# Kernel tuning notes

Hardware: AMD Instinct MI355X
Metric: run time of the kernel (lower is better)

The kernel has to match this reference:

```python
import jax, jax.numpy as jnp
import numpy as np

N = 50000      # num_nodes
E = 800000     # num_edges
D_IN = 128
D_HID = 128
D_EMB = 128
G = 4          # num_gcns
BN_EPS = 1e-5


def setup_inputs() -> dict:
    key = jax.random.key(0)
    ks = jax.random.split(key, 8)
    x = jax.random.normal(ks[0], (N, D_IN), dtype=jnp.float32)
    edge_index = jax.random.randint(ks[1], (2, E), 0, N, dtype=jnp.int64)
    # per-GCN params, stacked on leading G axis
    W1 = jax.random.normal(ks[2], (G, D_IN, D_HID), dtype=jnp.float32) / np.sqrt(D_IN)
    b1 = jnp.zeros((G, D_HID), dtype=jnp.float32)
    W2 = jax.random.normal(ks[3], (G, D_HID, D_EMB), dtype=jnp.float32) / np.sqrt(D_HID)
    b2 = jnp.zeros((G, D_EMB), dtype=jnp.float32)
    gamma1 = jnp.ones((G, D_HID), dtype=jnp.float32)
    beta1 = jnp.zeros((G, D_HID), dtype=jnp.float32)
    gamma2 = jnp.ones((G, D_EMB), dtype=jnp.float32)
    beta2 = jnp.zeros((G, D_EMB), dtype=jnp.float32)
    alpha = jnp.asarray(0.25, dtype=jnp.float32)  # PReLU (single shared param)
    mix_embed = jnp.full((N, G), 1.0 / G, dtype=jnp.float32)
    return {"x": x, "edge_index": edge_index, "W1": W1, "b1": b1, "W2": W2,
            "b2": b2, "gamma1": gamma1, "beta1": beta1, "gamma2": gamma2,
            "beta2": beta2, "alpha": alpha, "mix_embed": mix_embed}


def _gcn_norm(edge_index, num_nodes):
    # PyG GCNConv: add self-loops, symmetric normalization D^-1/2 (A+I) D^-1/2
    row, col = edge_index[0], edge_index[1]
    loop = jnp.arange(num_nodes, dtype=edge_index.dtype)
    row = jnp.concatenate([row, loop])
    col = jnp.concatenate([col, loop])
    w = jnp.ones(row.shape[0], dtype=jnp.float32)
    deg = jax.ops.segment_sum(w, col, num_segments=num_nodes)
    dinv = jnp.where(deg > 0, deg ** -0.5, 0.0)
    norm = dinv[row] * w * dinv[col]
    return row, col, norm


def _propagate(h, row, col, norm, num_nodes):
    # gather from source, scale by edge norm, scatter-add to target
    msg = h[row] * norm[:, None]
    return jax.ops.segment_sum(msg, col, num_segments=num_nodes)


def _batchnorm(z, gamma, beta):
    mu = jnp.mean(z, axis=0)
    var = jnp.mean((z - mu) ** 2, axis=0)  # biased, as torch BN training mode
    return (z - mu) * jax.lax.rsqrt(var + BN_EPS) * gamma + beta


def _prelu(z, alpha):
    return jnp.where(z > 0, z, alpha * z)


def reference(x, edge_index, W1, b1, W2, b2, gamma1, beta1, gamma2, beta2, alpha, mix_embed):
    num_nodes = x.shape[0]
    row, col, norm = _gcn_norm(edge_index, num_nodes)
    mix = jax.nn.softmax(mix_embed, axis=-1)  # [N, G]
    out = jnp.zeros((num_nodes, D_EMB), dtype=x.dtype)
    for g in range(G):  # small fixed number of mixture components
        h = x @ W1[g]
        z = _propagate(h, row, col, norm, num_nodes) + b1[g]
        z = _prelu(_batchnorm(z, gamma1[g], beta1[g]), alpha)
        h = z @ W2[g]
        z = _propagate(h, row, col, norm, num_nodes) + b2[g]
        z = _prelu(_batchnorm(z, gamma2[g], beta2[g]), alpha)
        out = out + mix[:, g:g + 1] * z
    return out
```

## Files before the change

kernel.cpp:

```cpp
#include <hip/hip_runtime.h>
#include <stdint.h>

static constexpr float EPS = 1e-5f;

typedef __attribute__((ext_vector_type(8))) short bfrag;
typedef __attribute__((ext_vector_type(4))) float ffrag;

__device__ __forceinline__ float bf2f(unsigned short u){
  union { unsigned int i; float f; } v; v.i = ((unsigned int)u) << 16; return v.f;
}
__device__ __forceinline__ unsigned short f2bf(float f){
  union { float f; unsigned int i; } v; v.f = f;
  unsigned int x = v.i;
  x += 0x7fffu + ((x >> 16) & 1u);
  return (unsigned short)(x >> 16);
}
__device__ __forceinline__ float lo16(unsigned int v){ return bf2f((unsigned short)(v & 0xffffu)); }
__device__ __forceinline__ float hi16(unsigned int v){ return bf2f((unsigned short)(v >> 16)); }
__device__ __forceinline__ unsigned int pack2(float a, float b){
  return ((unsigned int)f2bf(b) << 16) | (unsigned int)f2bf(a);
}

__global__ void k_deg(const int* __restrict__ col, int* __restrict__ indeg, int N, int E){
  int e = blockIdx.x * 256 + threadIdx.x;
  if (e < E){
    unsigned c = (unsigned)col[e];
    if (c < (unsigned)N) atomicAdd(&indeg[c], 1);
  }
}

__global__ void k_blocksum(const int* __restrict__ indeg, int* __restrict__ bsum, int N){
  __shared__ int sm[256];
  int i = blockIdx.x * 256 + threadIdx.x;
  sm[threadIdx.x] = (i < N) ? indeg[i] : 0;
  __syncthreads();
  for (int d = 128; d > 0; d >>= 1){
    if (threadIdx.x < d) sm[threadIdx.x] += sm[threadIdx.x + d];
    __syncthreads();
  }
  if (threadIdx.x == 0) bsum[blockIdx.x] = sm[0];
}

__global__ void k_scan_bsum(int* bsum, int nb){
  if (threadIdx.x == 0 && blockIdx.x == 0){
    int acc = 0;
    for (int b = 0; b < nb; b++){ int v = bsum[b]; bsum[b] = acc; acc += v; }
  }
}

__global__ void k_scan_node(const int* __restrict__ indeg, const int* __restrict__ bsum,
                            int* __restrict__ offs, int* __restrict__ cursor,
                            float* __restrict__ dinv, int N){
  __shared__ int sm[256];
  int i = blockIdx.x * 256 + threadIdx.x;
  int v = (i < N) ? indeg[i] : 0;
  sm[threadIdx.x] = v;
  __syncthreads();
  for (int d = 1; d < 256; d <<= 1){
    int t = (threadIdx.x >= d) ? sm[threadIdx.x - d] : 0;
    __syncthreads();
    sm[threadIdx.x] += t;
    __syncthreads();
  }
  if (i < N){
    int o = bsum[blockIdx.x] + sm[threadIdx.x] - v;
    offs[i] = o; cursor[i] = o;
    dinv[i] = rsqrtf((float)(v + 1));
  }
}

__global__ void k_scatter(const int* __restrict__ row, const int* __restrict__ col,
                          int* __restrict__ cursor, int* __restrict__ csr, int N, int E){
  int e = blockIdx.x * 256 + threadIdx.x;
  if (e < E){
    unsigned c = (unsigned)col[e];
    if (c < (unsigned)N){
      int p = atomicAdd(&cursor[c], 1);
      unsigned r = (unsigned)row[e];
      csr[p] = (r < (unsigned)N) ? (int)r : 0;
    }
  }
}

__global__ void k_wcast(const float* __restrict__ W, unsigned short* __restrict__ Wt, int total){
  int idx = blockIdx.x * 256 + threadIdx.x;
  if (idx < total){
    int c = idx >> 7, k = idx & 127;
    int g = c >> 7, j = c & 127;
    Wt[idx] = f2bf(W[(size_t)g*16384 + k*128 + j]);
  }
}

__global__ void k_castx(const float* __restrict__ x, const float* __restrict__ dinv,
                        unsigned short* __restrict__ xs, int total4){
  int idx = blockIdx.x * 256 + threadIdx.x;
  int stride = gridDim.x * 256;
  for (; idx < total4; idx += stride){
    int i = idx >> 5;
    float di = dinv[i];
    float4 v = ((const float4*)x)[idx];
    ushort4 o;
    o.x = f2bf(di * v.x); o.y = f2bf(di * v.y);
    o.z = f2bf(di * v.z); o.w = f2bf(di * v.w);
    ((ushort4*)xs)[idx] = o;
  }
}

__global__ __launch_bounds__(64) void k_prop_x(const unsigned int* __restrict__ xs2,
                                               const int* __restrict__ csr,
                                               const int* __restrict__ offs, const int* __restrict__ indeg,
                                               const float* __restrict__ dinv,
                                               unsigned int* __restrict__ s2, int N){
  int i = blockIdx.x;
  int c2 = threadIdx.x;
  unsigned int sv = xs2[(size_t)i*64 + c2];
  float ax = lo16(sv), ay = hi16(sv);
  int e = offs[i], end = e + indeg[i];
  for (; e + 4 <= end; e += 4){
    int r0 = csr[e], r1 = csr[e+1], r2 = csr[e+2], r3 = csr[e+3];
    unsigned int v0 = xs2[(size_t)r0*64 + c2];
    unsigned int v1 = xs2[(size_t)r1*64 + c2];
    unsigned int v2 = xs2[(size_t)r2*64 + c2];
    unsigned int v3 = xs2[(size_t)r3*64 + c2];
    ax += lo16(v0) + lo16(v1) + lo16(v2) + lo16(v3);
    ay += hi16(v0) + hi16(v1) + hi16(v2) + hi16(v3);
  }
  for (; e < end; e++){
    unsigned int v = xs2[(size_t)csr[e]*64 + c2];
    ax += lo16(v); ay += hi16(v);
  }
  float di = dinv[i];
  s2[(size_t)i*64 + c2] = pack2(di * ax, di * ay);
}

__global__ __launch_bounds__(256) void k_mm_mfma(const unsigned short* __restrict__ in,
                                                 const unsigned short* __restrict__ Wt,
                                                 const float* __restrict__ bias,
                                                 unsigned short* __restrict__ out,
                                                 int N, int in_stride, int kmul){
  int wave = threadIdx.x >> 6;
  int lane = threadIdx.x & 63;
  int l16 = lane & 15, quad = lane >> 4;
  int node = blockIdx.x * 16 + l16;
  int nc = node < N ? node : N - 1;
  int colbase0 = wave * 128;
  int kofs = kmul * wave;

  const unsigned short* inrow = in + (size_t)nc * in_stride + kofs + quad * 8;
  bfrag b0 = *(const bfrag*)(inrow);
  bfrag b1 = *(const bfrag*)(inrow + 32);
  bfrag b2 = *(const bfrag*)(inrow + 64);
  bfrag b3 = *(const bfrag*)(inrow + 96);

  #pragma unroll
  for (int ct = 0; ct < 8; ct++){
    int colbase = colbase0 + ct * 16;
    const unsigned short* wrow = Wt + (size_t)(colbase + l16) * 128 + quad * 8;
    bfrag a0 = *(const bfrag*)(wrow);
    bfrag a1 = *(const bfrag*)(wrow + 32);
    bfrag a2 = *(const bfrag*)(wrow + 64);
    bfrag a3 = *(const bfrag*)(wrow + 96);
    ffrag acc = {0.f, 0.f, 0.f, 0.f};
    acc = __builtin_amdgcn_mfma_f32_16x16x32_bf16(a0, b0, acc, 0, 0, 0);
    acc = __builtin_amdgcn_mfma_f32_16x16x32_bf16(a1, b1, acc, 0, 0, 0);
    acc = __builtin_amdgcn_mfma_f32_16x16x32_bf16(a2, b2, acc, 0, 0, 0);
    acc = __builtin_amdgcn_mfma_f32_16x16x32_bf16(a3, b3, acc, 0, 0, 0);
    float4 bb = *(const float4*)(bias + colbase + quad * 4);
    uint2 o;
    o.x = pack2(acc[0] + bb.x, acc[1] + bb.y);
    o.y = pack2(acc[2] + bb.z, acc[3] + bb.w);
    if (node < N)
      *(uint2*)(out + (size_t)node * 512 + colbase + quad * 4) = o;
  }
}

__global__ __launch_bounds__(256) void k_stats(const unsigned int* __restrict__ z2,
                                               float* __restrict__ ssum, float* __restrict__ ssq, int N){
  int t = threadIdx.x;
  int rpb = (N + gridDim.x - 1) / gridDim.x;
  int r0 = blockIdx.x * rpb;
  int r1 = min(N, r0 + rpb);
  float s0 = 0.f, q0 = 0.f, s1 = 0.f, q1 = 0.f;
  for (int r = r0; r < r1; r++){
    unsigned int v = z2[(size_t)r * 256 + t];
    float a = lo16(v), b = hi16(v);
    s0 += a; q0 += a * a; s1 += b; q1 += b * b;
  }
  atomicAdd(&ssum[2 * t], s0);     atomicAdd(&ssq[2 * t], q0);
  atomicAdd(&ssum[2 * t + 1], s1); atomicAdd(&ssq[2 * t + 1], q1);
}

__global__ void k_bnfix(const float* __restrict__ ssum, const float* __restrict__ ssq,
                        const float* __restrict__ gamma, const float* __restrict__ beta,
                        float* __restrict__ scale, float* __restrict__ shift, int N){
  int c = blockIdx.x * 256 + threadIdx.x;
  if (c < 512){
    float mean = ssum[c] / (float)N;
    float var  = ssq[c] / (float)N - mean * mean;
    float rstd = rsqrtf(var + EPS);
    float sc = rstd * gamma[c];
    scale[c] = sc;
    shift[c] = beta[c] - mean * sc;
  }
}

__global__ void k_h(const unsigned short* __restrict__ z, const float* __restrict__ scale,
                    const float* __restrict__ shift, const float* __restrict__ alpha_p,
                    const float* __restrict__ dinv,
                    unsigned short* __restrict__ h, int total4){
  float alpha = alpha_p[0];
  int idx = blockIdx.x * 256 + threadIdx.x;
  int stride = gridDim.x * 256;
  for (; idx < total4; idx += stride){
    ushort4 u = ((const ushort4*)z)[idx];
    int c4 = idx & 127;
    int i  = idx >> 7;
    float di = dinv[i];
    float4 sc = ((const float4*)scale)[c4];
    float4 sh = ((const float4*)shift)[c4];
    float a0 = bf2f(u.x)*sc.x + sh.x; a0 = a0 > 0.f ? a0 : alpha*a0;
    float a1 = bf2f(u.y)*sc.y + sh.y; a1 = a1 > 0.f ? a1 : alpha*a1;
    float a2 = bf2f(u.z)*sc.z + sh.z; a2 = a2 > 0.f ? a2 : alpha*a2;
    float a3 = bf2f(u.w)*sc.w + sh.w; a3 = a3 > 0.f ? a3 : alpha*a3;
    ushort4 o; o.x = f2bf(di*a0); o.y = f2bf(di*a1); o.z = f2bf(di*a2); o.w = f2bf(di*a3);
    ((ushort4*)h)[idx] = o;
  }
}

__global__ __launch_bounds__(256) void k_prop_h(const unsigned int* __restrict__ h2,
                                                const int* __restrict__ csr,
                                                const int* __restrict__ offs, const int* __restrict__ indeg,
                                                const float* __restrict__ dinv,
                                                unsigned int* __restrict__ t2, int N){
  int i = blockIdx.x;
  int c2 = threadIdx.x;
  unsigned int sv = h2[(size_t)i*256 + c2];
  float ax = lo16(sv), ay = hi16(sv);
  int e = offs[i], end = e + indeg[i];
  for (; e + 4 <= end; e += 4){
    int r0 = csr[e], r1 = csr[e+1], r2 = csr[e+2], r3 = csr[e+3];
    unsigned int v0 = h2[(size_t)r0*256 + c2];
    unsigned int v1 = h2[(size_t)r1*256 + c2];
    unsigned int v2 = h2[(size_t)r2*256 + c2];
    unsigned int v3 = h2[(size_t)r3*256 + c2];
    ax += lo16(v0) + lo16(v1) + lo16(v2) + lo16(v3);
    ay += hi16(v0) + hi16(v1) + hi16(v2) + hi16(v3);
  }
  for (; e < end; e++){
    unsigned int v = h2[(size_t)csr[e]*256 + c2];
    ax += lo16(v); ay += hi16(v);
  }
  float di = dinv[i];
  t2[(size_t)i*256 + c2] = pack2(di * ax, di * ay);
}

__global__ void k_out(const unsigned short* __restrict__ z2, const float* __restrict__ scale,
                      const float* __restrict__ shift, const float* __restrict__ mixe,
                      const float* __restrict__ alpha_p, float* __restrict__ out, int N){
  float alpha = alpha_p[0];
  int idx = blockIdx.x * 256 + threadIdx.x;
  if (idx >= N * 128) return;
  int i = idx >> 7, j = idx & 127;
  float4 me = ((const float4*)mixe)[i];
  float mx = fmaxf(fmaxf(me.x, me.y), fmaxf(me.z, me.w));
  float e0 = __expf(me.x - mx), e1 = __expf(me.y - mx), e2 = __expf(me.z - mx), e3 = __expf(me.w - mx);
  float inv = 1.f / (e0 + e1 + e2 + e3);
  float r = 0.f;
  #pragma unroll
  for (int g = 0; g < 4; g++){
    int c = g * 128 + j;
    float v = bf2f(z2[(size_t)i*512 + c]) * scale[c] + shift[c];
    v = v > 0.f ? v : alpha * v;
    float m = (g == 0) ? e0 : (g == 1) ? e1 : (g == 2) ? e2 : e3;
    r += m * inv * v;
  }
  out[idx] = r;
}

extern "C" void kernel_launch(void* const* d_in, const int* in_sizes, int n_in,
                              void* d_out, int out_size, void* d_ws, size_t ws_size,
                              hipStream_t stream) {
  const float* x      = (const float*)d_in[0];
  const int*   ei     = (const int*)d_in[1];
  const float* W1     = (const float*)d_in[2];
  const float* b1     = (const float*)d_in[3];
  const float* W2     = (const float*)d_in[4];
  const float* b2     = (const float*)d_in[5];
  const float* gamma1 = (const float*)d_in[6];
  const float* beta1  = (const float*)d_in[7];
  const float* gamma2 = (const float*)d_in[8];
  const float* beta2  = (const float*)d_in[9];
  const float* alpha  = (const float*)d_in[10];
  const float* mixe   = (const float*)d_in[11];
  float* out = (float*)d_out;

  const int N = in_sizes[0] / 128;
  const int E = in_sizes[1] / 2;
  const int* rowv = ei;
  const int* colv = ei + E;

  char* w = (char*)d_ws;
  size_t off = 0;
  auto take = [&](size_t bytes) -> void* {
    void* p = w + off;
    off = (off + bytes + 255) & ~(size_t)255;
    return p;
  };
  int*   indeg  = (int*)take((size_t)N * 4);
  int*   cursor = (int*)take((size_t)N * 4);
  int*   offs   = (int*)take((size_t)N * 4);
  int*   bsum   = (int*)take(4096);
  float* dinv   = (float*)take((size_t)N * 4);
  float* sum1   = (float*)take(2048);
  float* sq1    = (float*)take(2048);
  float* sum2   = (float*)take(2048);
  float* sq2    = (float*)take(2048);
  float* scale1 = (float*)take(2048);
  float* shift1 = (float*)take(2048);
  float* scale2 = (float*)take(2048);
  float* shift2 = (float*)take(2048);
  int*   csr    = (int*)take((size_t)E * 4);
  unsigned short* Wt1 = (unsigned short*)take(512 * 128 * 2);
  unsigned short* Wt2 = (unsigned short*)take(512 * 128 * 2);
  unsigned short* xs = (unsigned short*)take((size_t)N * 128 * 2);
  unsigned short* sb = (unsigned short*)take((size_t)N * 128 * 2);
  unsigned short* z  = (unsigned short*)take((size_t)N * 512 * 2);
  unsigned short* h  = (unsigned short*)take((size_t)N * 512 * 2);
  unsigned short* z2 = (unsigned short*)take((size_t)N * 512 * 2);

  hipMemsetAsync(indeg, 0, (size_t)N * 4, stream);
  hipMemsetAsync(sum1, 0, 4 * 2048, stream);

  int ebl = (E + 255) / 256;
  int nb  = (N + 255) / 256;

  k_deg<<<ebl, 256, 0, stream>>>(colv, indeg, N, E);
  k_blocksum<<<nb, 256, 0, stream>>>(indeg, bsum, N);
  k_scan_bsum<<<1, 64, 0, stream>>>(bsum, nb);
  k_scan_node<<<nb, 256, 0, stream>>>(indeg, bsum, offs, cursor, dinv, N);
  k_scatter<<<ebl, 256, 0, stream>>>(rowv, colv, cursor, csr, N, E);

  k_wcast<<<256, 256, 0, stream>>>(W1, Wt1, 512 * 128);
  k_wcast<<<256, 256, 0, stream>>>(W2, Wt2, 512 * 128);

  k_castx<<<512, 256, 0, stream>>>(x, dinv, xs, N * 32);
  k_prop_x<<<N, 64, 0, stream>>>((const unsigned int*)xs, csr, offs, indeg, dinv, (unsigned int*)sb, N);

  int mmb = (N + 15) / 16;
  k_mm_mfma<<<mmb, 256, 0, stream>>>(sb, Wt1, b1, z, N, 128, 0);
  k_stats<<<512, 256, 0, stream>>>((const unsigned int*)z, sum1, sq1, N);
  k_bnfix<<<2, 256, 0, stream>>>(sum1, sq1, gamma1, beta1, scale1, shift1, N);
  k_h<<<2048, 256, 0, stream>>>(z, scale1, shift1, alpha, dinv, h, N * 128);
  k_prop_h<<<N, 256, 0, stream>>>((const unsigned int*)h, csr, offs, indeg, dinv, (unsigned int*)z, N);
  k_mm_mfma<<<mmb, 256, 0, stream>>>(z, Wt2, b2, z2, N, 512, 128);
  k_stats<<<512, 256, 0, stream>>>((const unsigned int*)z2, sum2, sq2, N);
  k_bnfix<<<2, 256, 0, stream>>>(sum2, sq2, gamma2, beta2, scale2, shift2, N);
  k_out<<<(N * 128 + 255) / 256, 256, 0, stream>>>(z2, scale2, shift2, mixe, alpha, out, N);
}
```

Baseline: 624.1 us.

## Compute BatchNorm stats via input Gram matrices and fuse BN/PReLU into matmuls

BatchNorm statistics of z = s@W are now derived from the Gram matrix sᵀs and the column means of the propagated input, computed with MFMA, instead of materialising z and reducing over it. This lets the first matmul apply BN, PReLU and the dinv scale directly in its epilogue. The second matmul likewise fuses BN, PReLU and the softmax mixture sum into its epilogue, which removes the z/z2 intermediate buffers and the separate stats, h and out kernels. It also parallelises the block-offset scan, merges the two weight casts into one launch, packs four nodes per block in the x propagation, and unrolls the gather loops by 8. The trade-off is fp32 atomics on Gram matrices from only 32 blocks per group, and variance computed as E[x²]−mean², which is less numerically robust. Biases are dropped, which is exact here because BN removes any constant shift.

After: 600.9 us. -3.7%, faster.

```diff
diff --git a/kernel.cpp b/kernel.cpp
--- a/kernel.cpp
+++ b/kernel.cpp
@@ -41,11 +41,19 @@
   if (threadIdx.x == 0) bsum[blockIdx.x] = sm[0];
 }
 
-__global__ void k_scan_bsum(int* bsum, int nb){
-  if (threadIdx.x == 0 && blockIdx.x == 0){
-    int acc = 0;
-    for (int b = 0; b < nb; b++){ int v = bsum[b]; bsum[b] = acc; acc += v; }
-  }
+__global__ __launch_bounds__(1024) void k_scan_bsum(int* bsum, int nb){
+  __shared__ int sm[1024];
+  int t = threadIdx.x;
+  int v = (t < nb) ? bsum[t] : 0;
+  sm[t] = v;
+  __syncthreads();
+  for (int d = 1; d < 1024; d <<= 1){
+    int u = (t >= d) ? sm[t - d] : 0;
+    __syncthreads();
+    sm[t] += u;
+    __syncthreads();
+  }
+  if (t < nb) bsum[t] = sm[t] - v;
 }
 
 __global__ void k_scan_node(const int* __restrict__ indeg, const int* __restrict__ bsum,
@@ -82,13 +90,14 @@
   }
 }
 
-__global__ void k_wcast(const float* __restrict__ W, unsigned short* __restrict__ Wt, int total){
+__global__ void k_wcast(const float* __restrict__ W1, const float* __restrict__ W2,
+                        unsigned short* __restrict__ Wt1, unsigned short* __restrict__ Wt2){
   int idx = blockIdx.x * 256 + threadIdx.x;
-  if (idx < total){
-    int c = idx >> 7, k = idx & 127;
-    int g = c >> 7, j = c & 127;
-    Wt[idx] = f2bf(W[(size_t)g*16384 + k*128 + j]);
-  }
+  const float* W = W1; unsigned short* Wt = Wt1;
+  if (idx >= 65536){ idx -= 65536; W = W2; Wt = Wt2; }
+  int c = idx >> 7, k = idx & 127;
+  int g = c >> 7, j = c & 127;
+  Wt[(size_t)c * 128 + k] = f2bf(W[(size_t)g*16384 + k*128 + j]);
 }
 
 __global__ void k_castx(const float* __restrict__ x, const float* __restrict__ dinv,
@@ -106,24 +115,26 @@
   }
 }
 
-__global__ __launch_bounds__(64) void k_prop_x(const unsigned int* __restrict__ xs2,
+__global__ __launch_bounds__(256) void k_prop_x(const unsigned int* __restrict__ xs2,
                                                const int* __restrict__ csr,
                                                const int* __restrict__ offs, const int* __restrict__ indeg,
                                                const float* __restrict__ dinv,
                                                unsigned int* __restrict__ s2, int N){
-  int i = blockIdx.x;
-  int c2 = threadIdx.x;
+  int i = blockIdx.x * 4 + (threadIdx.x >> 6);
+  if (i >= N) return;
+  int c2 = threadIdx.x & 63;
   unsigned int sv = xs2[(size_t)i*64 + c2];
   float ax = lo16(sv), ay = hi16(sv);
   int e = offs[i], end = e + indeg[i];
-  for (; e + 4 <= end; e += 4){
+  for (; e + 8 <= end; e += 8){
     int r0 = csr[e], r1 = csr[e+1], r2 = csr[e+2], r3 = csr[e+3];
-    unsigned int v0 = xs2[(size_t)r0*64 + c2];
-    unsigned int v1 = xs2[(size_t)r1*64 + c2];
-    unsigned int v2 = xs2[(size_t)r2*64 + c2];
-    unsigned int v3 = xs2[(size_t)r3*64 + c2];
-    ax += lo16(v0) + lo16(v1) + lo16(v2) + lo16(v3);
-    ay += hi16(v0) + hi16(v1) + hi16(v2) + hi16(v3);
+    int r4 = csr[e+4], r5 = csr[e+5], r6 = csr[e+6], r7 = csr[e+7];
+    unsigned int v0 = xs2[(size_t)r0*64 + c2], v1 = xs2[(size_t)r1*64 + c2];
+    unsigned int v2 = xs2[(size_t)r2*64 + c2], v3 = xs2[(size_t)r3*64 + c2];
+    unsigned int v4 = xs2[(size_t)r4*64 + c2], v5 = xs2[(size_t)r5*64 + c2];
+    unsigned int v6 = xs2[(size_t)r6*64 + c2], v7 = xs2[(size_t)r7*64 + c2];
+    ax += lo16(v0)+lo16(v1)+lo16(v2)+lo16(v3)+lo16(v4)+lo16(v5)+lo16(v6)+lo16(v7);
+    ay += hi16(v0)+hi16(v1)+hi16(v2)+hi16(v3)+hi16(v4)+hi16(v5)+hi16(v6)+hi16(v7);
   }
   for (; e < end; e++){
     unsigned int v = xs2[(size_t)csr[e]*64 + c2];
@@ -133,20 +144,137 @@
   s2[(size_t)i*64 + c2] = pack2(di * ax, di * ay);
 }
 
-__global__ __launch_bounds__(256) void k_mm_mfma(const unsigned short* __restrict__ in,
-                                                 const unsigned short* __restrict__ Wt,
-                                                 const float* __restrict__ bias,
-                                                 unsigned short* __restrict__ out,
-                                                 int N, int in_stride, int kmul){
-  int wave = threadIdx.x >> 6;
-  int lane = threadIdx.x & 63;
+__global__ __launch_bounds__(256) void k_gram(const unsigned short* __restrict__ in,
+                                              int rstride, int coff128,
+                                              float* __restrict__ Gbase, float* __restrict__ msumbase,
+                                              int N){
+  int gy = blockIdx.y;
+  const unsigned short* src = in + gy * coff128;
+  float* G = Gbase + (size_t)gy * 16384;
+  float* msum = msumbase + gy * 128;
+
+  __shared__ unsigned short st[128 * 40];
+  __shared__ float colsum[128];
+
+  int t = threadIdx.x;
+  int wv = t >> 6, lane = t & 63, l16 = lane & 15, quad = lane >> 4;
+  if (t < 128) colsum[t] = 0.f;
+
+  int sn = t & 31, scb = t >> 5;
+
+  ffrag acc[2][8];
+  #pragma unroll
+  for (int a = 0; a < 2; a++)
+    #pragma unroll
+    for (int b = 0; b < 8; b++) acc[a][b] = (ffrag){0.f,0.f,0.f,0.f};
+
+  float cs[16];
+  #pragma unroll
+  for (int j = 0; j < 16; j++) cs[j] = 0.f;
+
+  for (int c0 = blockIdx.x * 32; c0 < N; c0 += gridDim.x * 32){
+    __syncthreads();
+    int n = c0 + sn;
+    ushort4 u0, u1, u2, u3;
+    if (n < N){
+      const ushort4* p = (const ushort4*)(src + (size_t)n * rstride + scb * 16);
+      u0 = p[0]; u1 = p[1]; u2 = p[2]; u3 = p[3];
+    } else {
+      u0 = u1 = u2 = u3 = (ushort4){0,0,0,0};
+    }
+    unsigned short vals[16] = {u0.x,u0.y,u0.z,u0.w, u1.x,u1.y,u1.z,u1.w,
+                               u2.x,u2.y,u2.z,u2.w, u3.x,u3.y,u3.z,u3.w};
+    #pragma unroll
+    for (int j = 0; j < 16; j++){
+      st[(scb * 16 + j) * 40 + sn] = vals[j];
+      cs[j] += bf2f(vals[j]);
+    }
+    __syncthreads();
+    #pragma unroll
+    for (int ta = 0; ta < 2; ta++){
+      int ra = wv * 2 + ta;
+      bfrag af = *(const bfrag*)&st[(ra * 16 + l16) * 40 + quad * 8];
+      #pragma unroll
+      for (int tb = 0; tb < 8; tb++){
+        bfrag bf = *(const bfrag*)&st[(tb * 16 + l16) * 40 + quad * 8];
+        acc[ta][tb] = __builtin_amdgcn_mfma_f32_16x16x32_bf16(af, bf, acc[ta][tb], 0, 0, 0);
+      }
+    }
+  }
+  #pragma unroll
+  for (int j = 0; j < 16; j++) atomicAdd(&colsum[scb * 16 + j], cs[j]);
+  __syncthreads();
+  if (t < 128) atomicAdd(&msum[t], colsum[t]);
+  #pragma unroll
+  for (int ta = 0; ta < 2; ta++){
+    #pragma unroll
+    for (int tb = 0; tb < 8; tb++){
+      int row0 = wv * 32 + ta * 16 + quad * 4;
+      int colg = tb * 16 + l16;
+      #pragma unroll
+      for (int r = 0; r < 4; r++)
+        atomicAdd(&G[(size_t)(row0 + r) * 128 + colg], acc[ta][tb][r]);
+    }
+  }
+}
+
+__global__ __launch_bounds__(64) void k_bnfit(const float* __restrict__ W,
+                                              const float* __restrict__ gamma, const float* __restrict__ beta,
+                                              const float* __restrict__ Gbase, int gmul,
+                                              const float* __restrict__ msumbase, int mmul,
+                                              float* __restrict__ scale, float* __restrict__ shiftF,
+                                              float invN){
+  int c = blockIdx.x;
+  int g = c >> 7, j = c & 127;
+  const float* Wc = W + (size_t)g * 16384 + j;
+  const float* G  = Gbase + (size_t)g * gmul;
+  const float* mv = msumbase + g * mmul;
+  __shared__ float wl[128];
+  __shared__ float ml[128];
+  int t = threadIdx.x;
+  for (int k = t; k < 128; k += 64){ wl[k] = Wc[(size_t)k * 128]; ml[k] = mv[k] * invN; }
+  __syncthreads();
+  float quad = 0.f, dm = 0.f;
+  #pragma unroll
+  for (int kk = 0; kk < 2; kk++){
+    int k = t + kk * 64;
+    float wk = wl[k];
+    dm += ml[k] * wk;
+    const float* Gr = G + (size_t)k * 128;
+    float p = 0.f;
+    for (int jj = 0; jj < 128; jj += 4){
+      float4 gg = *(const float4*)(Gr + jj);
+      float4 ww = *(const float4*)(wl + jj);
+      p += gg.x*ww.x + gg.y*ww.y + gg.z*ww.z + gg.w*ww.w;
+    }
+    quad += wk * p;
+  }
+  for (int o = 32; o > 0; o >>= 1){
+    quad += __shfl_down(quad, o);
+    dm   += __shfl_down(dm, o);
+  }
+  if (t == 0){
+    float var = quad * invN - dm * dm;
+    float sc = gamma[c] * rsqrtf(var + EPS);
+    scale[c] = sc;
+    shiftF[c] = beta[c] - dm * sc;
+  }
+}
+
+__global__ __launch_bounds__(256) void k_mm1f(const unsigned short* __restrict__ in,
+                                              const unsigned short* __restrict__ Wt,
+                                              const float* __restrict__ scale, const float* __restrict__ shiftF,
+                                              const float* __restrict__ alpha_p, const float* __restrict__ dinv,
+                                              unsigned short* __restrict__ h, int N){
+  float alpha = alpha_p[0];
+  int wave = threadIdx.x >> 6, lane = threadIdx.x & 63;
   int l16 = lane & 15, quad = lane >> 4;
   int node = blockIdx.x * 16 + l16;
   int nc = node < N ? node : N - 1;
   int colbase0 = wave * 128;
-  int kofs = kmul * wave;
-
-  const unsigned short* inrow = in + (size_t)nc * in_stride + kofs + quad * 8;
+  float di = dinv[nc];
+
+  const unsigned short* inrow = in + (size_t)nc * 128 + quad * 8;
   bfrag b0 = *(const bfrag*)(inrow);
   bfrag b1 = *(const bfrag*)(inrow + 32);
   bfrag b2 = *(const bfrag*)(inrow + 64);
@@ -165,65 +293,18 @@
     acc = __builtin_amdgcn_mfma_f32_16x16x32_bf16(a1, b1, acc, 0, 0, 0);
     acc = __builtin_amdgcn_mfma_f32_16x16x32_bf16(a2, b2, acc, 0, 0, 0);
     acc = __builtin_amdgcn_mfma_f32_16x16x32_bf16(a3, b3, acc, 0, 0, 0);
-    float4 bb = *(const float4*)(bias + colbase + quad * 4);
+    int cb = colbase + quad * 4;
+    float4 sc = *(const float4*)(scale + cb);
+    float4 sh = *(const float4*)(shiftF + cb);
+    float v0 = acc[0]*sc.x + sh.x; v0 = v0 > 0.f ? v0 : alpha*v0;
+    float v1 = acc[1]*sc.y + sh.y; v1 = v1 > 0.f ? v1 : alpha*v1;
+    float v2 = acc[2]*sc.z + sh.z; v2 = v2 > 0.f ? v2 : alpha*v2;
+    float v3 = acc[3]*sc.w + sh.w; v3 = v3 > 0.f ? v3 : alpha*v3;
     uint2 o;
-    o.x = pack2(acc[0] + bb.x, acc[1] + bb.y);
-    o.y = pack2(acc[2] + bb.z, acc[3] + bb.w);
+    o.x = pack2(di*v0, di*v1);
+    o.y = pack2(di*v2, di*v3);
     if (node < N)
-      *(uint2*)(out + (size_t)node * 512 + colbase + quad * 4) = o;
-  }
-}
-
-__global__ __launch_bounds__(256) void k_stats(const unsigned int* __restrict__ z2,
-                                               float* __restrict__ ssum, float* __restrict__ ssq, int N){
-  int t = threadIdx.x;
-  int rpb = (N + gridDim.x - 1) / gridDim.x;
-  int r0 = blockIdx.x * rpb;
-  int r1 = min(N, r0 + rpb);
-  float s0 = 0.f, q0 = 0.f, s1 = 0.f, q1 = 0.f;
-  for (int r = r0; r < r1; r++){
-    unsigned int v = z2[(size_t)r * 256 + t];
-    float a = lo16(v), b = hi16(v);
-    s0 += a; q0 += a * a; s1 += b; q1 += b * b;
-  }
-  atomicAdd(&ssum[2 * t], s0);     atomicAdd(&ssq[2 * t], q0);
-  atomicAdd(&ssum[2 * t + 1], s1); atomicAdd(&ssq[2 * t + 1], q1);
-}
-
-__global__ void k_bnfix(const float* __restrict__ ssum, const float* __restrict__ ssq,
-                        const float* __restrict__ gamma, const float* __restrict__ beta,
-                        float* __restrict__ scale, float* __restrict__ shift, int N){
-  int c = blockIdx.x * 256 + threadIdx.x;
-  if (c < 512){
-    float mean = ssum[c] / (float)N;
-    float var  = ssq[c] / (float)N - mean * mean;
-    float rstd = rsqrtf(var + EPS);
-    float sc = rstd * gamma[c];
-    scale[c] = sc;
-    shift[c] = beta[c] - mean * sc;
-  }
-}
-
-__global__ void k_h(const unsigned short* __restrict__ z, const float* __restrict__ scale,
-                    const float* __restrict__ shift, const float* __restrict__ alpha_p,
-                    const float* __restrict__ dinv,
-                    unsigned short* __restrict__ h, int total4){
-  float alpha = alpha_p[0];
-  int idx = blockIdx.x * 256 + threadIdx.x;
-  int stride = gridDim.x * 256;
-  for (; idx < total4; idx += stride){
-    ushort4 u = ((const ushort4*)z)[idx];
-    int c4 = idx & 127;
-    int i  = idx >> 7;
-    float di = dinv[i];
-    float4 sc = ((const float4*)scale)[c4];
-    float4 sh = ((const float4*)shift)[c4];
-    float a0 = bf2f(u.x)*sc.x + sh.x; a0 = a0 > 0.f ? a0 : alpha*a0;
-    float a1 = bf2f(u.y)*sc.y + sh.y; a1 = a1 > 0.f ? a1 : alpha*a1;
-    float a2 = bf2f(u.z)*sc.z + sh.z; a2 = a2 > 0.f ? a2 : alpha*a2;
-    float a3 = bf2f(u.w)*sc.w + sh.w; a3 = a3 > 0.f ? a3 : alpha*a3;
-    ushort4 o; o.x = f2bf(di*a0); o.y = f2bf(di*a1); o.z = f2bf(di*a2); o.w = f2bf(di*a3);
-    ((ushort4*)h)[idx] = o;
+      *(uint2*)(h + (size_t)node * 512 + cb) = o;
   }
 }
 
@@ -237,14 +318,15 @@
   unsigned int sv = h2[(size_t)i*256 + c2];
   float ax = lo16(sv), ay = hi16(sv);
   int e = offs[i], end = e + indeg[i];
-  for (; e + 4 <= end; e += 4){
+  for (; e + 8 <= end; e += 8){
     int r0 = csr[e], r1 = csr[e+1], r2 = csr[e+2], r3 = csr[e+3];
-    unsigned int v0 = h2[(size_t)r0*256 + c2];
-    unsigned int v1 = h2[(size_t)r1*256 + c2];
-    unsigned int v2 = h2[(size_t)r2*256 + c2];
-    unsigned int v3 = h2[(size_t)r3*256 + c2];
-    ax += lo16(v0) + lo16(v1) + lo16(v2) + lo16(v3);
-    ay += hi16(v0) + hi16(v1) + hi16(v2) + hi16(v3);
+    int r4 = csr[e+4], r5 = csr[e+5], r6 = csr[e+6], r7 = csr[e+7];
+    unsigned int v0 = h2[(size_t)r0*256 + c2], v1 = h2[(size_t)r1*256 + c2];
+    unsigned int v2 = h2[(size_t)r2*256 + c2], v3 = h2[(size_t)r3*256 + c2];
+    unsigned int v4 = h2[(size_t)r4*256 + c2], v5 = h2[(size_t)r5*256 + c2];
+    unsigned int v6 = h2[(size_t)r6*256 + c2], v7 = h2[(size_t)r7*256 + c2];
+    ax += lo16(v0)+lo16(v1)+lo16(v2)+lo16(v3)+lo16(v4)+lo16(v5)+lo16(v6)+lo16(v7);
+    ay += hi16(v0)+hi16(v1)+hi16(v2)+hi16(v3)+hi16(v4)+hi16(v5)+hi16(v6)+hi16(v7);
   }
   for (; e < end; e++){
     unsigned int v = h2[(size_t)csr[e]*256 + c2];
@@ -254,27 +336,71 @@
   t2[(size_t)i*256 + c2] = pack2(di * ax, di * ay);
 }
 
-__global__ void k_out(const unsigned short* __restrict__ z2, const float* __restrict__ scale,
-                      const float* __restrict__ shift, const float* __restrict__ mixe,
-                      const float* __restrict__ alpha_p, float* __restrict__ out, int N){
+__global__ __launch_bounds__(256) void k_mm2f(const unsigned short* __restrict__ t,
+                                              const unsigned short* __restrict__ Wt,
+                                              const float* __restrict__ scale, const float* __restrict__ shiftF,
+                                              const float* __restrict__ alpha_p, const float* __restrict__ mixe,
+                                              float* __restrict__ out, int N){
+  __shared__ float red[4][16][132];
   float alpha = alpha_p[0];
-  int idx = blockIdx.x * 256 + threadIdx.x;
-  if (idx >= N * 128) return;
-  int i = idx >> 7, j = idx & 127;
-  float4 me = ((const float4*)mixe)[i];
+  int wave = threadIdx.x >> 6, lane = threadIdx.x & 63;
+  int l16 = lane & 15, quad = lane >> 4;
+  int node = blockIdx.x * 16 + l16;
+  int nc = node < N ? node : N - 1;
+
+  float4 me = ((const float4*)mixe)[nc];
   float mx = fmaxf(fmaxf(me.x, me.y), fmaxf(me.z, me.w));
   float e0 = __expf(me.x - mx), e1 = __expf(me.y - mx), e2 = __expf(me.z - mx), e3 = __expf(me.w - mx);
   float inv = 1.f / (e0 + e1 + e2 + e3);
-  float r = 0.f;
-  #pragma unroll
-  for (int g = 0; g < 4; g++){
-    int c = g * 128 + j;
-    float v = bf2f(z2[(size_t)i*512 + c]) * scale[c] + shift[c];
-    v = v > 0.f ? v : alpha * v;
-    float m = (g == 0) ? e0 : (g == 1) ? e1 : (g == 2) ? e2 : e3;
-    r += m * inv * v;
-  }
-  out[idx] = r;
+  float wvx = ((wave == 0) ? e0 : (wave == 1) ? e1 : (wave == 2) ? e2 : e3) * inv;
+
+  const unsigned short* inrow = t + (size_t)nc * 512 + wave * 128 + quad * 8;
+  bfrag b0 = *(const bfrag*)(inrow);
+  bfrag b1 = *(const bfrag*)(inrow + 32);
+  bfrag b2 = *(const bfrag*)(inrow + 64);
+  bfrag b3 = *(const bfrag*)(inrow + 96);
+
+  #pragma unroll
+  for (int ct = 0; ct < 8; ct++){
+    int c512 = wave * 128 + ct * 16;
+    const unsigned short* wrow = Wt + (size_t)(c512 + l16) * 128 + quad * 8;
+    bfrag a0 = *(const bfrag*)(wrow);
+    bfrag a1 = *(const bfrag*)(wrow + 32);
+    bfrag a2 = *(const bfrag*)(wrow + 64);
+    bfrag a3 = *(const bfrag*)(wrow + 96);
+    ffrag acc = {0.f, 0.f, 0.f, 0.f};
+    acc = __builtin_amdgcn_mfma_f32_16x16x32_bf16(a0, b0, acc, 0, 0, 0);
+    acc = __builtin_amdgcn_mfma_f32_16x16x32_bf16(a1, b1, acc, 0, 0, 0);
+    acc = __builtin_amdgcn_mfma_f32_16x16x32_bf16(a2, b2, acc, 0, 0, 0);
+    acc = __builtin_amdgcn_mfma_f32_16x16x32_bf16(a3, b3, acc, 0, 0, 0);
+    int cb = c512 + quad * 4;
+    float4 sc = *(const float4*)(scale + cb);
+    float4 sh = *(const float4*)(shiftF + cb);
+    float v0 = acc[0]*sc.x + sh.x; v0 = v0 > 0.f ? v0 : alpha*v0;
+    float v1 = acc[1]*sc.y + sh.y; v1 = v1 > 0.f ? v1 : alpha*v1;
+    float v2 = acc[2]*sc.z + sh.z; v2 = v2 > 0.f ? v2 : alpha*v2;
+    float v3 = acc[3]*sc.w + sh.w; v3 = v3 > 0.f ? v3 : alpha*v3;
+    int j = ct * 16 + quad * 4;
+    float4 wr = {wvx*v0, wvx*v1, wvx*v2, wvx*v3};
+    *(float4*)&red[wave][l16][j] = wr;
+  }
+  __syncthreads();
+  int tt = threadIdx.x;
+  int nn = tt >> 4, j0 = (tt & 15) * 8;
+  int gnode = blockIdx.x * 16 + nn;
+  if (gnode < N){
+    float4 r0 = {0,0,0,0}, r1 = {0,0,0,0};
+    #pragma unroll
+    for (int w = 0; w < 4; w++){
+      float4 p0 = *(const float4*)&red[w][nn][j0];
+      float4 p1 = *(const float4*)&red[w][nn][j0 + 4];
+      r0.x += p0.x; r0.y += p0.y; r0.z += p0.z; r0.w += p0.w;
+      r1.x += p1.x; r1.y += p1.y; r1.z += p1.z; r1.w += p1.w;
+    }
+    float* op = out + (size_t)gnode * 128 + j0;
+    *(float4*)(op) = r0;
+    *(float4*)(op + 4) = r1;
+  }
 }
 
 extern "C" void kernel_launch(void* const* d_in, const int* in_sizes, int n_in,
@@ -293,6 +419,7 @@
   const float* alpha  = (const float*)d_in[10];
   const float* mixe   = (const float*)d_in[11];
   float* out = (float*)d_out;
+  (void)b1; (void)b2;
 
   const int N = in_sizes[0] / 128;
   const int E = in_sizes[1] / 2;
@@ -311,10 +438,10 @@
   int*   offs   = (int*)take((size_t)N * 4);
   int*   bsum   = (int*)take(4096);
   float* dinv   = (float*)take((size_t)N * 4);
-  float* sum1   = (float*)take(2048);
-  float* sq1    = (float*)take(2048);
-  float* sum2   = (float*)take(2048);
-  float* sq2    = (float*)take(2048);
+  float* G1     = (float*)take(65536);
+  float* G2     = (float*)take(262144);
+  float* m1     = (float*)take(512);
+  float* m2     = (float*)take(2048);
   float* scale1 = (float*)take(2048);
   float* shift1 = (float*)take(2048);
   float* scale2 = (float*)take(2048);
@@ -324,36 +451,33 @@
   unsigned short* Wt2 = (unsigned short*)take(512 * 128 * 2);
   unsigned short* xs = (unsigned short*)take((size_t)N * 128 * 2);
   unsigned short* sb = (unsigned short*)take((size_t)N * 128 * 2);
-  unsigned short* z  = (unsigned short*)take((size_t)N * 512 * 2);
   unsigned short* h  = (unsigned short*)take((size_t)N * 512 * 2);
-  unsigned short* z2 = (unsigned short*)take((size_t)N * 512 * 2);
+  unsigned short* tb = (unsigned short*)take((size_t)N * 512 * 2);
 
   hipMemsetAsync(indeg, 0, (size_t)N * 4, stream);
-  hipMemsetAsync(sum1, 0, 4 * 2048, stream);
+  hipMemsetAsync(G1, 0, 65536 + 262144 + 512 + 2048, stream);
 
   int ebl = (E + 255) / 256;
   int nb  = (N + 255) / 256;
+  float invN = 1.0f / (float)N;
 
   k_deg<<<ebl, 256, 0, stream>>>(colv, indeg, N, E);
   k_blocksum<<<nb, 256, 0, stream>>>(indeg, bsum, N);
-  k_scan_bsum<<<1, 64, 0, stream>>>(bsum, nb);
+  k_scan_bsum<<<1, 1024, 0, stream>>>(bsum, nb);
   k_scan_node<<<nb, 256, 0, stream>>>(indeg, bsum, offs, cursor, dinv, N);
   k_scatter<<<ebl, 256, 0, stream>>>(rowv, colv, cursor, csr, N, E);
 
-  k_wcast<<<256, 256, 0, stream>>>(W1, Wt1, 512 * 128);
-  k_wcast<<<256, 256, 0, stream>>>(W2, Wt2, 512 * 128);
-
+  k_wcast<<<512, 256, 0, stream>>>(W1, W2, Wt1, Wt2);
   k_castx<<<512, 256, 0, stream>>>(x, dinv, xs, N * 32);
-  k_prop_x<<<N, 64, 0, stream>>>((const unsigned int*)xs, csr, offs, indeg, dinv, (unsigned int*)sb, N);
-
-  int mmb = (N + 15) / 16;
-  k_mm_mfma<<<mmb, 256, 0, stream>>>(sb, Wt1, b1, z, N, 128, 0);
-  k_stats<<<512, 256, 0, stream>>>((const unsigned int*)z, sum1, sq1, N);
-  k_bnfix<<<2, 256, 0, stream>>>(sum1, sq1, gamma1, beta1, scale1, shift1, N);
-  k_h<<<2048, 256, 0, stream>>>(z, scale1, shift1, alpha, dinv, h, N * 128);
-  k_prop_h<<<N, 256, 0, stream>>>((const unsigned int*)h, csr, offs, indeg, dinv, (unsigned int*)z, N);
-  k_mm_mfma<<<mmb, 256, 0, stream>>>(z, Wt2, b2, z2, N, 512, 128);
-  k_stats<<<512, 256, 0, stream>>>((const unsigned int*)z2, sum2, sq2, N);
-  k_bnfix<<<2, 256, 0, stream>>>(sum2, sq2, gamma2, beta2, scale2, shift2, N);
-  k_out<<<(N * 128 + 255) / 256, 256, 0, stream>>>(z2, scale2, shift2, mixe, alpha, out, N);
-}
+  k_prop_x<<<(N + 3) / 4, 256, 0, stream>>>((const unsigned int*)xs, csr, offs, indeg, dinv, (unsigned int*)sb, N);
+
+  k_gram<<<dim3(32, 1), 256, 0, stream>>>(sb, 128, 0, G1, m1, N);
+  k_bnfit<<<512, 64, 0, stream>>>(W1, gamma1, beta1, G1, 0, m1, 0, scale1, shift1, invN);
+  k_mm1f<<<(N + 15) / 16, 256, 0, stream>>>(sb, Wt1, scale1, shift1, alpha, dinv, h, N);
+
+  k_prop_h<<<N, 256, 0, stream>>>((const unsigned int*)h, csr, offs, indeg, dinv, (unsigned int*)tb, N);
+
+  k_gram<<<dim3(32, 4), 256, 0, stream>>>(tb, 512, 128, G2, m2, N);
+  k_bnfit<<<512, 64, 0, stream>>>(W2, gamma2, beta2, G2, 16384, m2, 128, scale2, shift2, invN);
+  k_mm2f<<<(N + 15) / 16, 256, 0, stream>>>(tb, Wt2, scale2, shift2, alpha, mixe, out, N);
+}
```
